# Kernel tuning notes

Hardware: AMD Instinct MI355X
Metric: run time of the kernel (lower is better)

The kernel has to match this reference:

```python
import jax, jax.numpy as jnp
import numpy as np

E = 1_600_000      # num edges
N = 50_000         # num nodes
G = 100            # num graphs in batch
EMB = 128          # emb_size
OUT = 256          # out_emb_size
NRAD = 6           # num_radial
NDENSE = 3         # num_dense


def setup_inputs() -> dict:
    key = jax.random.key(0)
    ks = jax.random.split(key, 8)
    m = jax.random.normal(ks[0], (E, EMB), dtype=jnp.float32)
    rbf = jax.random.normal(ks[1], (E, NRAD), dtype=jnp.float32)
    src = jax.random.randint(ks[2], (E,), 0, N, dtype=jnp.int64)
    graph_ids = jnp.sort(jax.random.randint(ks[3], (N,), 0, G, dtype=jnp.int64))
    # parameters (torch Linear convention: W [out, in])
    W_rbf = jax.random.normal(ks[4], (EMB, NRAD), dtype=jnp.float32) / np.sqrt(NRAD)
    W_up = jax.random.normal(ks[5], (OUT, EMB), dtype=jnp.float32) / np.sqrt(EMB)
    W_dense = jax.random.normal(ks[6], (NDENSE, OUT, OUT), dtype=jnp.float32) / np.sqrt(OUT)
    b_dense = jnp.zeros((NDENSE, OUT), dtype=jnp.float32)
    return {"m": m, "rbf": rbf, "src": src, "graph_ids": graph_ids,
            "W_rbf": W_rbf, "W_up": W_up, "W_dense": W_dense, "b_dense": b_dense}


def reference(m, rbf, src, graph_ids, W_rbf, W_up, W_dense, b_dense):
    # edge transform: tmp = m * dense_rbf(rbf)            [E, EMB]
    tmp = m * jnp.einsum('er,fr->ef', rbf, W_rbf)
    # reverse-graph copy_e/sum == scatter-sum onto original src nodes
    t = jax.ops.segment_sum(tmp, src, num_segments=N)     # [N, EMB]
    # up projection (no bias)
    t = jnp.einsum('ne,oe->no', t, W_up)                  # [N, OUT]
    # dense MLP with SiLU
    for i in range(NDENSE):
        t = jax.nn.silu(jnp.einsum('no,po->np', t, W_dense[i]) + b_dense[i])
    # extensive readout: per-graph sum
    out = jax.ops.segment_sum(t, graph_ids, num_segments=G)  # [G, OUT]
    return out
```

## Files before the change

### kernel.cpp

```cpp
#include <hip/hip_runtime.h>
#include <hip/hip_bf16.h>

typedef __attribute__((ext_vector_type(8))) short short8;
typedef __attribute__((ext_vector_type(4))) float f32x4;

#define EMB 128
#define OUT 256
#define NRAD 6
#define NDENSE 3
#define BSH 7
#define MAXBKT 512
#define HB 256

static __device__ __forceinline__ unsigned short f32_to_bf16(float f) {
    union { float f; unsigned u; } v; v.f = f;
    unsigned r = v.u + 0x7fffu + ((v.u >> 16) & 1u);
    return (unsigned short)(r >> 16);
}
static __device__ __forceinline__ float bf16_to_f32(unsigned short h) {
    union { unsigned u; float f; } v; v.u = ((unsigned)h) << 16;
    return v.f;
}
static __device__ __forceinline__ float silu(float x) {
    return x / (1.f + __expf(-x));
}
static __device__ __forceinline__ void gload_lds16(const void* gp, void* lp) {
    __builtin_amdgcn_global_load_lds(
        (const __attribute__((address_space(1))) void*)gp,
        (__attribute__((address_space(3))) void*)lp, 16, 0, 0);
}

__global__ __launch_bounds__(256) void init_kernel(
        const float* __restrict__ Wup, const float* __restrict__ Wd,
        unsigned short* __restrict__ Wbf, float* __restrict__ out, int outn) {
    int i = blockIdx.x * blockDim.x + threadIdx.x;
    int stride = gridDim.x * blockDim.x;
    for (int j = i; j < outn; j += stride) out[j] = 0.f;
    const int n1 = OUT * EMB, n2 = NDENSE * OUT * OUT;
    for (int j = i; j < n1 + n2; j += stride)
        Wbf[j] = f32_to_bf16(j < n1 ? Wup[j] : Wd[j - n1]);
}

__global__ __launch_bounds__(256) void bhist_kernel(
        const int* __restrict__ src, int* __restrict__ bpart, int E, int nbkt) {
    __shared__ int h[MAXBKT];
    for (int b = threadIdx.x; b < nbkt; b += 256) h[b] = 0;
    __syncthreads();
    int stride = gridDim.x * blockDim.x;
    for (int e = blockIdx.x * blockDim.x + threadIdx.x; e < E; e += stride)
        atomicAdd(&h[src[e] >> BSH], 1);
    __syncthreads();
    int* row = bpart + (size_t)blockIdx.x * MAXBKT;
    for (int b = threadIdx.x; b < nbkt; b += 256) row[b] = h[b];
}

__global__ __launch_bounds__(512) void bscan_kernel(
        const int* __restrict__ bpart, int* __restrict__ bbase,
        int* __restrict__ gcursor, int nbkt, int E) {
    __shared__ int s[MAXBKT];
    int t = threadIdx.x;
    int v = 0;
    if (t < nbkt)
        for (int k = 0; k < HB; ++k) v += bpart[(size_t)k * MAXBKT + t];
    s[t] = v;
    __syncthreads();
    for (int d = 1; d < MAXBKT; d <<= 1) {
        int x = (t >= d) ? s[t - d] : 0;
        __syncthreads();
        s[t] += x;
        __syncthreads();
    }
    if (t < nbkt) {
        int ex = s[t] - v;
        bbase[t] = ex;
        gcursor[t] = ex;
    }
    if (t == 0) bbase[nbkt] = E;
}

__global__ __launch_bounds__(256) void bscatter_kernel(
        const int* __restrict__ src, int* __restrict__ gcursor,
        int2* __restrict__ pairs, int E, int nbkt) {
    __shared__ int h[MAXBKT];
    __shared__ int base[MAXBKT];
    for (int b = threadIdx.x; b < nbkt; b += 256) h[b] = 0;
    __syncthreads();
    const int per = (E + gridDim.x - 1) / gridDim.x;
    const int e0 = blockIdx.x * per;
    const int e1 = min(e0 + per, E);
    for (int e = e0 + threadIdx.x; e < e1; e += 256)
        atomicAdd(&h[src[e] >> BSH], 1);
    __syncthreads();
    for (int b = threadIdx.x; b < nbkt; b += 256)
        base[b] = h[b] ? atomicAdd(&gcursor[b], h[b]) : 0;
    __syncthreads();
    for (int e = e0 + threadIdx.x; e < e1; e += 256) {
        int s = src[e];
        int pos = atomicAdd(&base[s >> BSH], 1);
        pairs[pos] = make_int2(e, s);
    }
}

__global__ __launch_bounds__(256) void local_csr_kernel(
        const int2* __restrict__ pairs, const int* __restrict__ bbase,
        int* __restrict__ offsets, int* __restrict__ perm, int N, int E, int nbkt) {
    __shared__ int cnt[128], exc[128], cur[128];
    const int b = blockIdx.x;
    const int t = threadIdx.x;
    const int n0 = b << BSH;
    const int nn = min(128, N - n0);
    const int p0 = bbase[b], p1 = bbase[b + 1];
    if (t < 128) cnt[t] = 0;
    __syncthreads();
    for (int i = p0 + t; i < p1; i += 256)
        atomicAdd(&cnt[pairs[i].y - n0], 1);
    __syncthreads();
    if (t < 128) exc[t] = cnt[t];
    __syncthreads();
    for (int d = 1; d < 128; d <<= 1) {
        int x = (t >= d && t < 128) ? exc[t - d] : 0;
        __syncthreads();
        if (t < 128) exc[t] += x;
        __syncthreads();
    }
    if (t < 128) {
        int ex = exc[t] - cnt[t];
        cur[t] = ex;
        if (t < nn) offsets[n0 + t] = p0 + ex;
    }
    if (b == 0 && t == 0) offsets[N] = E;
    __syncthreads();
    for (int i = p0 + t; i < p1; i += 256) {
        int2 pr = pairs[i];
        int pos = p0 + atomicAdd(&cur[pr.y - n0], 1);
        perm[pos] = pr.x;
    }
}

__global__ __launch_bounds__(256) void edge_accum_kernel(
        const float* __restrict__ m, const float* __restrict__ rbf,
        const int* __restrict__ perm, const int* __restrict__ offsets,
        const float* __restrict__ W_rbf, uint2* __restrict__ t_pack, int N) {
    const int lane = threadIdx.x & 63;
    const int h = lane >> 5;
    const int c = lane & 31;
    const int gw = blockIdx.x * (blockDim.x >> 6) + (threadIdx.x >> 6);
    const int nwaves = gridDim.x * (blockDim.x >> 6);

    float wk[4][6];
#pragma unroll
    for (int k = 0; k < 4; ++k)
#pragma unroll
        for (int j = 0; j < 6; ++j) wk[k][j] = W_rbf[(4 * c + k) * NRAD + j];

    for (int node = gw; node < N; node += nwaves) {
        const int beg = offsets[node], end = offsets[node + 1];
        float a0 = 0.f, a1 = 0.f, a2 = 0.f, a3 = 0.f;
        int pe = 0;
        if (beg < end) {
            int pi = beg + (lane & 15); if (pi > end - 1) pi = end - 1;
            pe = perm[pi];
        }
        for (int cb = beg; cb < end; cb += 16) {
            int pe_next = 0;
            if (cb + 16 < end) {
                int pi = cb + 16 + (lane & 15); if (pi > end - 1) pi = end - 1;
                pe_next = perm[pi];
            }
#pragma unroll
            for (int p = 0; p < 8; ++p) {
                int e = __shfl(pe, 2 * p + h);
                const float2* rp = (const float2*)(rbf + (size_t)e * NRAD);
                float2 r0 = rp[0], r1 = rp[1], r2 = rp[2];
                float4 mv = *(const float4*)(m + (size_t)e * EMB + 4 * c);
                float g = (cb + 2 * p + h < end) ? 1.f : 0.f;
                float p0 = (wk[0][0]*r0.x + wk[0][1]*r0.y + wk[0][2]*r1.x
                          + wk[0][3]*r1.y + wk[0][4]*r2.x + wk[0][5]*r2.y) * g;
                float p1 = (wk[1][0]*r0.x + wk[1][1]*r0.y + wk[1][2]*r1.x
                          + wk[1][3]*r1.y + wk[1][4]*r2.x + wk[1][5]*r2.y) * g;
                float p2 = (wk[2][0]*r0.x + wk[2][1]*r0.y + wk[2][2]*r1.x
                          + wk[2][3]*r1.y + wk[2][4]*r2.x + wk[2][5]*r2.y) * g;
                float p3 = (wk[3][0]*r0.x + wk[3][1]*r0.y + wk[3][2]*r1.x
                          + wk[3][3]*r1.y + wk[3][4]*r2.x + wk[3][5]*r2.y) * g;
                a0 = fmaf(mv.x, p0, a0);
                a1 = fmaf(mv.y, p1, a1);
                a2 = fmaf(mv.z, p2, a2);
                a3 = fmaf(mv.w, p3, a3);
            }
            pe = pe_next;
        }
        a0 += __shfl_xor(a0, 32);
        a1 += __shfl_xor(a1, 32);
        a2 += __shfl_xor(a2, 32);
        a3 += __shfl_xor(a3, 32);
        if (h == 0) {
            uint2 pk;
            pk.x = (unsigned)f32_to_bf16(a0) | ((unsigned)f32_to_bf16(a1) << 16);
            pk.y = (unsigned)f32_to_bf16(a2) | ((unsigned)f32_to_bf16(a3) << 16);
            t_pack[(size_t)node * 32 + c] = pk;
        }
    }
}

template<int K, int ACT>
__global__ __launch_bounds__(256) void gemm2_kernel(
        const unsigned short* __restrict__ A, const unsigned short* __restrict__ W,
        const float* __restrict__ bias, unsigned short* __restrict__ C, int M) {
    __shared__ char lds[32768];
    char* As = lds;
    char* Ws = lds + 16384;

    const int w    = threadIdx.x >> 6;
    const int lane = threadIdx.x & 63;
    const int r    = lane & 15;
    const int g    = lane >> 4;
    const int wr   = w >> 1;
    const int wc   = w & 1;
    const int row0 = blockIdx.x * 128;
    const int col0 = blockIdx.y * 128;

    f32x4 acc[4][4];
#pragma unroll
    for (int i = 0; i < 4; ++i)
#pragma unroll
        for (int j = 0; j < 4; ++j) acc[i][j] = (f32x4){0.f, 0.f, 0.f, 0.f};

    const int lrow = (lane >> 3);
    const int cdst = (lane & 7) * 16;

    for (int kc = 0; kc < K; kc += 64) {
        if (kc) __syncthreads();
#pragma unroll
        for (int it = 0; it < 4; ++it) {
            int slot = it * 4 + w;
            int row  = slot * 8 + lrow;
            int csrc = cdst ^ ((row & 7) << 4);
            int ga   = row0 + row; if (ga >= M) ga = M - 1;
            gload_lds16((const char*)A + ((size_t)ga * K + kc) * 2 + csrc,
                        As + slot * 1024);
            int gw_  = col0 + row;
            gload_lds16((const char*)W + ((size_t)gw_ * K + kc) * 2 + csrc,
                        Ws + slot * 1024);
        }
        asm volatile("s_waitcnt vmcnt(0)" ::: "memory");
        __syncthreads();

#pragma unroll
        for (int ks = 0; ks < 2; ++ks) {
            short8 af[4], bf[4];
#pragma unroll
            for (int mi = 0; mi < 4; ++mi) {
                int row = wr * 64 + mi * 16 + r;
                int byte = row * 128 + ks * 64 + g * 16;
                byte ^= (r & 7) << 4;
                af[mi] = *(const short8*)(As + byte);
            }
#pragma unroll
            for (int nj = 0; nj < 4; ++nj) {
                int col = wc * 64 + nj * 16 + r;
                int byte = col * 128 + ks * 64 + g * 16;
                byte ^= (r & 7) << 4;
                bf[nj] = *(const short8*)(Ws + byte);
            }
#pragma unroll
            for (int mi = 0; mi < 4; ++mi)
#pragma unroll
                for (int nj = 0; nj < 4; ++nj)
                    acc[mi][nj] = __builtin_amdgcn_mfma_f32_16x16x32_bf16(
                        af[mi], bf[nj], acc[mi][nj], 0, 0, 0);
        }
    }

#pragma unroll
    for (int nj = 0; nj < 4; ++nj) {
        int gcol = col0 + wc * 64 + nj * 16 + r;
        float b = bias ? bias[gcol] : 0.f;
#pragma unroll
        for (int mi = 0; mi < 4; ++mi) {
#pragma unroll
            for (int q = 0; q < 4; ++q) {
                int grow = row0 + wr * 64 + mi * 16 + g * 4 + q;
                if (grow < M) {
                    float x = acc[mi][nj][q] + b;
                    if (ACT) x = silu(x);
                    C[(size_t)grow * OUT + gcol] = f32_to_bf16(x);
                }
            }
        }
    }
}

__global__ __launch_bounds__(256) void graph_partial_kernel(
        const unsigned short* __restrict__ h, const int* __restrict__ gids,
        float* __restrict__ out, int M) {
    int gph = blockIdx.x, s = blockIdx.y;
    int c = threadIdx.x;
    int lo = 0, hi = M;
    while (lo < hi) { int mid = (lo + hi) >> 1; if (gids[mid] < gph) lo = mid + 1; else hi = mid; }
    int lo2 = lo, hi2 = M;
    while (lo2 < hi2) { int mid = (lo2 + hi2) >> 1; if (gids[mid] < gph + 1) lo2 = mid + 1; else hi2 = mid; }
    int len = lo2 - lo;
    int q = (len + 3) >> 2;
    int b0 = lo + s * q;
    int b1 = b0 + q; if (b1 > lo2) b1 = lo2;
    float a0 = 0.f, a1 = 0.f;
    int n = b0;
    for (; n + 1 < b1; n += 2) {
        a0 += bf16_to_f32(h[(size_t)n * OUT + c]);
        a1 += bf16_to_f32(h[(size_t)(n + 1) * OUT + c]);
    }
    for (; n < b1; ++n) a0 += bf16_to_f32(h[(size_t)n * OUT + c]);
    float v = a0 + a1;
    if (b0 < b1) atomicAdd(&out[(size_t)gph * OUT + c], v);
}

extern "C" void kernel_launch(void* const* d_in, const int* in_sizes, int n_in,
                              void* d_out, int out_size, void* d_ws, size_t ws_size,
                              hipStream_t stream) {
    const float* m         = (const float*)d_in[0];
    const float* rbf       = (const float*)d_in[1];
    const int*   src       = (const int*)d_in[2];
    const int*   gids      = (const int*)d_in[3];
    const float* W_rbf     = (const float*)d_in[4];
    const float* W_up      = (const float*)d_in[5];
    const float* W_dense   = (const float*)d_in[6];
    const float* b_dense   = (const float*)d_in[7];
    float* out = (float*)d_out;

    const int E = in_sizes[2];
    const int N = in_sizes[3];
    const int G = out_size / OUT;
    const int nbkt = (N + 127) >> BSH;

    size_t off = 0;
    auto alloc = [&](size_t bytes) -> void* {
        void* p = (char*)d_ws + off;
        off += (bytes + 255) & ~(size_t)255;
        return p;
    };
    int* bpart   = (int*)alloc((size_t)HB * MAXBKT * 4);
    int* bbase   = (int*)alloc((size_t)(MAXBKT + 1) * 4);
    int* gcursor = (int*)alloc((size_t)MAXBKT * 4);
    int* offsets = (int*)alloc(((size_t)N + 1) * 4);
    int2* pairs  = (int2*)alloc((size_t)E * 8);
    int* perm    = (int*)alloc((size_t)E * 4);
    unsigned short* t_bf = (unsigned short*)alloc((size_t)N * EMB * 2);
    unsigned short* h0   = (unsigned short*)alloc((size_t)N * OUT * 2);
    unsigned short* h1   = (unsigned short*)alloc((size_t)N * OUT * 2);
    unsigned short* Wbf  = (unsigned short*)alloc((size_t)(OUT * EMB + NDENSE * OUT * OUT) * 2);
    unsigned short* Wup_bf = Wbf;
    unsigned short* Wd_bf  = Wbf + OUT * EMB;

    bhist_kernel<<<HB, 256, 0, stream>>>(src, bpart, E, nbkt);
    init_kernel<<<512, 256, 0, stream>>>(W_up, W_dense, Wbf, out, out_size);
    bscan_kernel<<<1, MAXBKT, 0, stream>>>(bpart, bbase, gcursor, nbkt, E);
    bscatter_kernel<<<512, 256, 0, stream>>>(src, gcursor, pairs, E, nbkt);
    local_csr_kernel<<<nbkt, 256, 0, stream>>>(pairs, bbase, offsets, perm, N, E, nbkt);

    edge_accum_kernel<<<2048, 256, 0, stream>>>(m, rbf, perm, offsets, W_rbf,
                                                (uint2*)t_bf, N);

    dim3 ggrid((N + 127) / 128, 2);
    gemm2_kernel<EMB, 0><<<ggrid, 256, 0, stream>>>(t_bf, Wup_bf, nullptr, h0, N);
    gemm2_kernel<OUT, 1><<<ggrid, 256, 0, stream>>>(h0, Wd_bf + 0 * OUT * OUT, b_dense + 0 * OUT, h1, N);
    gemm2_kernel<OUT, 1><<<ggrid, 256, 0, stream>>>(h1, Wd_bf + 1 * OUT * OUT, b_dense + 1 * OUT, h0, N);
    gemm2_kernel<OUT, 1><<<ggrid, 256, 0, stream>>>(h0, Wd_bf + 2 * OUT * OUT, b_dense + 2 * OUT, h1, N);

    graph_partial_kernel<<<dim3(G, 4), 256, 0, stream>>>(h1, gids, out, N);
}
```

Measured before the change: 450.8 us.

## Fuse local CSR build and edge accumulation into bucketed LDS-atomic accumulation

Replaces the per-bucket CSR construction and the per-node gather-accumulate kernel with one kernel per 128-node bucket. Each block walks that bucket's (edge, src) pairs and accumulates m*rbf-projection into a 64 KB shared-memory tile using LDS float atomics, then writes bf16 results. This drops the perm/offsets arrays and a kernel launch, at the cost of only 391 blocks with large LDS (low occupancy, under 2 waves per CU) and atomic contention. It also unrolls the bucket-scan reduction loop.

```diff
diff --git a/kernel.cpp b/kernel.cpp
--- a/kernel.cpp
+++ b/kernel.cpp
@@ -60,8 +60,10 @@
     __shared__ int s[MAXBKT];
     int t = threadIdx.x;
     int v = 0;
-    if (t < nbkt)
+    if (t < nbkt) {
+#pragma unroll 8
         for (int k = 0; k < HB; ++k) v += bpart[(size_t)k * MAXBKT + t];
+    }
     s[t] = v;
     __syncthreads();
     for (int d = 1; d < MAXBKT; d <<= 1) {
@@ -101,104 +103,64 @@
     }
 }
 
-__global__ __launch_bounds__(256) void local_csr_kernel(
+__global__ __launch_bounds__(256) void bucket_accum_kernel(
+        const float* __restrict__ m, const float* __restrict__ rbf,
         const int2* __restrict__ pairs, const int* __restrict__ bbase,
-        int* __restrict__ offsets, int* __restrict__ perm, int N, int E, int nbkt) {
-    __shared__ int cnt[128], exc[128], cur[128];
+        const float* __restrict__ W_rbf, uint2* __restrict__ t_pack, int N) {
+    __shared__ float acc[128 * 128];
+    const int t = threadIdx.x;
     const int b = blockIdx.x;
-    const int t = threadIdx.x;
     const int n0 = b << BSH;
     const int nn = min(128, N - n0);
     const int p0 = bbase[b], p1 = bbase[b + 1];
-    if (t < 128) cnt[t] = 0;
-    __syncthreads();
-    for (int i = p0 + t; i < p1; i += 256)
-        atomicAdd(&cnt[pairs[i].y - n0], 1);
-    __syncthreads();
-    if (t < 128) exc[t] = cnt[t];
-    __syncthreads();
-    for (int d = 1; d < 128; d <<= 1) {
-        int x = (t >= d && t < 128) ? exc[t - d] : 0;
-        __syncthreads();
-        if (t < 128) exc[t] += x;
-        __syncthreads();
-    }
-    if (t < 128) {
-        int ex = exc[t] - cnt[t];
-        cur[t] = ex;
-        if (t < nn) offsets[n0 + t] = p0 + ex;
-    }
-    if (b == 0 && t == 0) offsets[N] = E;
-    __syncthreads();
-    for (int i = p0 + t; i < p1; i += 256) {
-        int2 pr = pairs[i];
-        int pos = p0 + atomicAdd(&cur[pr.y - n0], 1);
-        perm[pos] = pr.x;
-    }
-}
-
-__global__ __launch_bounds__(256) void edge_accum_kernel(
-        const float* __restrict__ m, const float* __restrict__ rbf,
-        const int* __restrict__ perm, const int* __restrict__ offsets,
-        const float* __restrict__ W_rbf, uint2* __restrict__ t_pack, int N) {
-    const int lane = threadIdx.x & 63;
-    const int h = lane >> 5;
-    const int c = lane & 31;
-    const int gw = blockIdx.x * (blockDim.x >> 6) + (threadIdx.x >> 6);
-    const int nwaves = gridDim.x * (blockDim.x >> 6);
+    const int c  = t & 31;
+    const int g8 = t >> 5;
+
+    for (int i = t; i < 128 * 128; i += 256) acc[i] = 0.f;
 
     float wk[4][6];
 #pragma unroll
     for (int k = 0; k < 4; ++k)
 #pragma unroll
-        for (int j = 0; j < 6; ++j) wk[k][j] = W_rbf[(4 * c + k) * NRAD + j];
-
-    for (int node = gw; node < N; node += nwaves) {
-        const int beg = offsets[node], end = offsets[node + 1];
-        float a0 = 0.f, a1 = 0.f, a2 = 0.f, a3 = 0.f;
-        int pe = 0;
-        if (beg < end) {
-            int pi = beg + (lane & 15); if (pi > end - 1) pi = end - 1;
-            pe = perm[pi];
-        }
-        for (int cb = beg; cb < end; cb += 16) {
-            int pe_next = 0;
-            if (cb + 16 < end) {
-                int pi = cb + 16 + (lane & 15); if (pi > end - 1) pi = end - 1;
-                pe_next = perm[pi];
+        for (int j = 0; j < 6; ++j) wk[k][j] = W_rbf[(c + 32 * k) * NRAD + j];
+    __syncthreads();
+
+    for (int i = p0; i < p1; i += 32) {
+        int2 pr[4]; float2 r[4][3]; float mv[4][4]; bool val[4];
+#pragma unroll
+        for (int u = 0; u < 4; ++u) {
+            int idx = i + u * 8 + g8;
+            val[u] = idx < p1;
+            int2 p = val[u] ? pairs[idx] : make_int2(0, n0);
+            pr[u] = p;
+            const float2* rp = (const float2*)(rbf + (size_t)p.x * NRAD);
+            r[u][0] = rp[0]; r[u][1] = rp[1]; r[u][2] = rp[2];
+            const float* mrow = m + (size_t)p.x * EMB;
+#pragma unroll
+            for (int k = 0; k < 4; ++k) mv[u][k] = mrow[c + 32 * k];
+        }
+#pragma unroll
+        for (int u = 0; u < 4; ++u) {
+            if (!val[u]) continue;
+            float* arow = acc + (pr[u].y - n0) * 128;
+#pragma unroll
+            for (int k = 0; k < 4; ++k) {
+                float p = wk[k][0]*r[u][0].x + wk[k][1]*r[u][0].y
+                        + wk[k][2]*r[u][1].x + wk[k][3]*r[u][1].y
+                        + wk[k][4]*r[u][2].x + wk[k][5]*r[u][2].y;
+                atomicAdd(&arow[c + 32 * k], mv[u][k] * p);
             }
-#pragma unroll
-            for (int p = 0; p < 8; ++p) {
-                int e = __shfl(pe, 2 * p + h);
-                const float2* rp = (const float2*)(rbf + (size_t)e * NRAD);
-                float2 r0 = rp[0], r1 = rp[1], r2 = rp[2];
-                float4 mv = *(const float4*)(m + (size_t)e * EMB + 4 * c);
-                float g = (cb + 2 * p + h < end) ? 1.f : 0.f;
-                float p0 = (wk[0][0]*r0.x + wk[0][1]*r0.y + wk[0][2]*r1.x
-                          + wk[0][3]*r1.y + wk[0][4]*r2.x + wk[0][5]*r2.y) * g;
-                float p1 = (wk[1][0]*r0.x + wk[1][1]*r0.y + wk[1][2]*r1.x
-                          + wk[1][3]*r1.y + wk[1][4]*r2.x + wk[1][5]*r2.y) * g;
-                float p2 = (wk[2][0]*r0.x + wk[2][1]*r0.y + wk[2][2]*r1.x
-                          + wk[2][3]*r1.y + wk[2][4]*r2.x + wk[2][5]*r2.y) * g;
-                float p3 = (wk[3][0]*r0.x + wk[3][1]*r0.y + wk[3][2]*r1.x
-                          + wk[3][3]*r1.y + wk[3][4]*r2.x + wk[3][5]*r2.y) * g;
-                a0 = fmaf(mv.x, p0, a0);
-                a1 = fmaf(mv.y, p1, a1);
-                a2 = fmaf(mv.z, p2, a2);
-                a3 = fmaf(mv.w, p3, a3);
-            }
-            pe = pe_next;
-        }
-        a0 += __shfl_xor(a0, 32);
-        a1 += __shfl_xor(a1, 32);
-        a2 += __shfl_xor(a2, 32);
-        a3 += __shfl_xor(a3, 32);
-        if (h == 0) {
-            uint2 pk;
-            pk.x = (unsigned)f32_to_bf16(a0) | ((unsigned)f32_to_bf16(a1) << 16);
-            pk.y = (unsigned)f32_to_bf16(a2) | ((unsigned)f32_to_bf16(a3) << 16);
-            t_pack[(size_t)node * 32 + c] = pk;
-        }
+        }
+    }
+    __syncthreads();
+
+    for (int idx = t; idx < nn * 32; idx += 256) {
+        int node = idx >> 5, cc = idx & 31;
+        const float* ap = acc + node * 128 + 4 * cc;
+        uint2 pk;
+        pk.x = (unsigned)f32_to_bf16(ap[0]) | ((unsigned)f32_to_bf16(ap[1]) << 16);
+        pk.y = (unsigned)f32_to_bf16(ap[2]) | ((unsigned)f32_to_bf16(ap[3]) << 16);
+        t_pack[(size_t)(n0 + node) * 32 + cc] = pk;
     }
 }
 
@@ -341,9 +303,7 @@
     int* bpart   = (int*)alloc((size_t)HB * MAXBKT * 4);
     int* bbase   = (int*)alloc((size_t)(MAXBKT + 1) * 4);
     int* gcursor = (int*)alloc((size_t)MAXBKT * 4);
-    int* offsets = (int*)alloc(((size_t)N + 1) * 4);
     int2* pairs  = (int2*)alloc((size_t)E * 8);
-    int* perm    = (int*)alloc((size_t)E * 4);
     unsigned short* t_bf = (unsigned short*)alloc((size_t)N * EMB * 2);
     unsigned short* h0   = (unsigned short*)alloc((size_t)N * OUT * 2);
     unsigned short* h1   = (unsigned short*)alloc((size_t)N * OUT * 2);
@@ -355,10 +315,9 @@
     init_kernel<<<512, 256, 0, stream>>>(W_up, W_dense, Wbf, out, out_size);
     bscan_kernel<<<1, MAXBKT, 0, stream>>>(bpart, bbase, gcursor, nbkt, E);
     bscatter_kernel<<<512, 256, 0, stream>>>(src, gcursor, pairs, E, nbkt);
-    local_csr_kernel<<<nbkt, 256, 0, stream>>>(pairs, bbase, offsets, perm, N, E, nbkt);
-
-    edge_accum_kernel<<<2048, 256, 0, stream>>>(m, rbf, perm, offsets, W_rbf,
-                                                (uint2*)t_bf, N);
+
+    bucket_accum_kernel<<<nbkt, 256, 0, stream>>>(m, rbf, pairs, bbase, W_rbf,
+                                                  (uint2*)t_bf, N);
 
     dim3 ggrid((N + 127) / 128, 2);
     gemm2_kernel<EMB, 0><<<ggrid, 256, 0, stream>>>(t_bf, Wup_bf, nullptr, h0, N);
```

After: 1.592 ms. +253.2%, slower.

## Fuse up-projection and dense MLP GEMMs into one kernel keeping activations in LDS

Applied to the files above, without the earlier changes.

Replaces the four separate GEMM launches (up projection plus three dense SiLU layers) with a single kernel. Each block owns 64 rows and keeps the full 256-wide intermediate activation in LDS across all layers, streaming only the weights. This removes the global writes and reads of the N×256 bf16 intermediates and three launches, but reloads every weight matrix per 64-row block and has no load/compute overlap. The bscan reduction loop is also given an unroll pragma.

```diff
diff --git a/kernel.cpp b/kernel.cpp
--- a/kernel.cpp
+++ b/kernel.cpp
@@ -60,8 +60,10 @@
     __shared__ int s[MAXBKT];
     int t = threadIdx.x;
     int v = 0;
-    if (t < nbkt)
+    if (t < nbkt) {
+#pragma unroll 8
         for (int k = 0; k < HB; ++k) v += bpart[(size_t)k * MAXBKT + t];
+    }
     s[t] = v;
     __syncthreads();
     for (int d = 1; d < MAXBKT; d <<= 1) {
@@ -202,65 +204,66 @@
     }
 }
 
-template<int K, int ACT>
-__global__ __launch_bounds__(256) void gemm2_kernel(
-        const unsigned short* __restrict__ A, const unsigned short* __restrict__ W,
-        const float* __restrict__ bias, unsigned short* __restrict__ C, int M) {
-    __shared__ char lds[32768];
-    char* As = lds;
-    char* Ws = lds + 16384;
-
-    const int w    = threadIdx.x >> 6;
-    const int lane = threadIdx.x & 63;
+__global__ __launch_bounds__(256) void fused_mlp2_kernel(
+        const unsigned short* __restrict__ A0,
+        const unsigned short* __restrict__ Wup,
+        const unsigned short* __restrict__ Wd,
+        const float* __restrict__ bd,
+        unsigned short* __restrict__ Hout, int M) {
+    __shared__ char Abuf[32768];
+    __shared__ char Wbuf[32768];
+    const int t    = threadIdx.x;
+    const int w    = t >> 6;
+    const int lane = t & 63;
     const int r    = lane & 15;
     const int g    = lane >> 4;
-    const int wr   = w >> 1;
-    const int wc   = w & 1;
-    const int row0 = blockIdx.x * 128;
-    const int col0 = blockIdx.y * 128;
+    const int row0 = blockIdx.x * 64;
 
     f32x4 acc[4][4];
+
+#pragma unroll
+    for (int it = 0; it < 4; ++it) {
+        int unit = it * 256 + t;
+        int row  = unit >> 4;
+        int seg  = unit & 15;
+        int csrc = (seg * 16) ^ ((row & 7) << 4);
+        int ga = row0 + row; if (ga >= M) ga = M - 1;
+        gload_lds16((const char*)A0 + (size_t)ga * 256 + csrc, Abuf + unit * 16);
+    }
+
 #pragma unroll
     for (int i = 0; i < 4; ++i)
 #pragma unroll
         for (int j = 0; j < 4; ++j) acc[i][j] = (f32x4){0.f, 0.f, 0.f, 0.f};
-
-    const int lrow = (lane >> 3);
-    const int cdst = (lane & 7) * 16;
-
-    for (int kc = 0; kc < K; kc += 64) {
-        if (kc) __syncthreads();
-#pragma unroll
-        for (int it = 0; it < 4; ++it) {
-            int slot = it * 4 + w;
-            int row  = slot * 8 + lrow;
-            int csrc = cdst ^ ((row & 7) << 4);
-            int ga   = row0 + row; if (ga >= M) ga = M - 1;
-            gload_lds16((const char*)A + ((size_t)ga * K + kc) * 2 + csrc,
-                        As + slot * 1024);
-            int gw_  = col0 + row;
-            gload_lds16((const char*)W + ((size_t)gw_ * K + kc) * 2 + csrc,
-                        Ws + slot * 1024);
+#pragma unroll
+    for (int kci = 0; kci < 2; ++kci) {
+        const int kc = kci * 64;
+        if (kci) __syncthreads();
+#pragma unroll
+        for (int it = 0; it < 8; ++it) {
+            int unit = it * 256 + t;
+            int wrow = unit >> 3;
+            int seg  = unit & 7;
+            int csrc = (seg * 16) ^ ((wrow & 7) << 4);
+            gload_lds16((const char*)Wup + (size_t)wrow * 256 + kc * 2 + csrc,
+                        Wbuf + unit * 16);
         }
         asm volatile("s_waitcnt vmcnt(0)" ::: "memory");
         __syncthreads();
-
 #pragma unroll
         for (int ks = 0; ks < 2; ++ks) {
             short8 af[4], bf[4];
 #pragma unroll
             for (int mi = 0; mi < 4; ++mi) {
-                int row = wr * 64 + mi * 16 + r;
-                int byte = row * 128 + ks * 64 + g * 16;
-                byte ^= (r & 7) << 4;
-                af[mi] = *(const short8*)(As + byte);
+                int row = mi * 16 + r;
+                int off = kc * 2 + ks * 64 + g * 16;
+                af[mi] = *(const short8*)(Abuf + row * 256 + (off ^ ((row & 7) << 4)));
             }
 #pragma unroll
             for (int nj = 0; nj < 4; ++nj) {
-                int col = wc * 64 + nj * 16 + r;
-                int byte = col * 128 + ks * 64 + g * 16;
-                byte ^= (r & 7) << 4;
-                bf[nj] = *(const short8*)(Ws + byte);
+                int col = w * 64 + nj * 16 + r;
+                bf[nj] = *(const short8*)(Wbuf + col * 128
+                          + ((ks * 64 + g * 16) ^ ((col & 7) << 4)));
             }
 #pragma unroll
             for (int mi = 0; mi < 4; ++mi)
@@ -270,21 +273,96 @@
                         af[mi], bf[nj], acc[mi][nj], 0, 0, 0);
         }
     }
-
-#pragma unroll
-    for (int nj = 0; nj < 4; ++nj) {
-        int gcol = col0 + wc * 64 + nj * 16 + r;
-        float b = bias ? bias[gcol] : 0.f;
-#pragma unroll
-        for (int mi = 0; mi < 4; ++mi) {
+    __syncthreads();
+#pragma unroll
+    for (int mi = 0; mi < 4; ++mi)
+#pragma unroll
+        for (int nj = 0; nj < 4; ++nj)
 #pragma unroll
             for (int q = 0; q < 4; ++q) {
-                int grow = row0 + wr * 64 + mi * 16 + g * 4 + q;
-                if (grow < M) {
-                    float x = acc[mi][nj][q] + b;
-                    if (ACT) x = silu(x);
-                    C[(size_t)grow * OUT + gcol] = f32_to_bf16(x);
+                int row = mi * 16 + g * 4 + q;
+                int col = w * 64 + nj * 16 + r;
+                *(unsigned short*)(Abuf + row * 512 + ((col * 2) ^ ((row & 7) << 4)))
+                    = f32_to_bf16(acc[mi][nj][q]);
+            }
+    __syncthreads();
+
+    for (int ell = 0; ell < NDENSE; ++ell) {
+        const unsigned short* Wl = Wd + (size_t)ell * OUT * OUT;
+        const float* bias = bd + ell * OUT;
+#pragma unroll
+        for (int i = 0; i < 4; ++i)
+#pragma unroll
+            for (int j = 0; j < 4; ++j) acc[i][j] = (f32x4){0.f, 0.f, 0.f, 0.f};
+#pragma unroll
+        for (int kci = 0; kci < 4; ++kci) {
+            const int kc = kci * 64;
+            __syncthreads();
+#pragma unroll
+            for (int it = 0; it < 8; ++it) {
+                int unit = it * 256 + t;
+                int wrow = unit >> 3;
+                int seg  = unit & 7;
+                int csrc = (seg * 16) ^ ((wrow & 7) << 4);
+                gload_lds16((const char*)Wl + (size_t)wrow * 512 + kc * 2 + csrc,
+                            Wbuf + unit * 16);
+            }
+            asm volatile("s_waitcnt vmcnt(0)" ::: "memory");
+            __syncthreads();
+#pragma unroll
+            for (int ks = 0; ks < 2; ++ks) {
+                short8 af[4], bf[4];
+#pragma unroll
+                for (int mi = 0; mi < 4; ++mi) {
+                    int row = mi * 16 + r;
+                    int off = kc * 2 + ks * 64 + g * 16;
+                    af[mi] = *(const short8*)(Abuf + row * 512 + (off ^ ((row & 7) << 4)));
                 }
+#pragma unroll
+                for (int nj = 0; nj < 4; ++nj) {
+                    int col = w * 64 + nj * 16 + r;
+                    bf[nj] = *(const short8*)(Wbuf + col * 128
+                              + ((ks * 64 + g * 16) ^ ((col & 7) << 4)));
+                }
+#pragma unroll
+                for (int mi = 0; mi < 4; ++mi)
+#pragma unroll
+                    for (int nj = 0; nj < 4; ++nj)
+                        acc[mi][nj] = __builtin_amdgcn_mfma_f32_16x16x32_bf16(
+                            af[mi], bf[nj], acc[mi][nj], 0, 0, 0);
+            }
+        }
+        __syncthreads();
+        if (ell < NDENSE - 1) {
+#pragma unroll
+            for (int mi = 0; mi < 4; ++mi)
+#pragma unroll
+                for (int nj = 0; nj < 4; ++nj) {
+                    int col = w * 64 + nj * 16 + r;
+                    float b = bias[col];
+#pragma unroll
+                    for (int q = 0; q < 4; ++q) {
+                        int row = mi * 16 + g * 4 + q;
+                        *(unsigned short*)(Abuf + row * 512
+                            + ((col * 2) ^ ((row & 7) << 4)))
+                            = f32_to_bf16(silu(acc[mi][nj][q] + b));
+                    }
+                }
+            __syncthreads();
+        } else {
+#pragma unroll
+            for (int nj = 0; nj < 4; ++nj) {
+                int gcol = w * 64 + nj * 16 + r;
+                float b = bias[gcol];
+#pragma unroll
+                for (int mi = 0; mi < 4; ++mi)
+#pragma unroll
+                    for (int q = 0; q < 4; ++q) {
+                        int grow = row0 + mi * 16 + g * 4 + q;
+                        if (grow < M)
+                            Hout[(size_t)grow * OUT + gcol]
+                                = f32_to_bf16(silu(acc[mi][nj][q] + b));
+                    }
             }
         }
     }
@@ -345,7 +423,6 @@
     int2* pairs  = (int2*)alloc((size_t)E * 8);
     int* perm    = (int*)alloc((size_t)E * 4);
     unsigned short* t_bf = (unsigned short*)alloc((size_t)N * EMB * 2);
-    unsigned short* h0   = (unsigned short*)alloc((size_t)N * OUT * 2);
     unsigned short* h1   = (unsigned short*)alloc((size_t)N * OUT * 2);
     unsigned short* Wbf  = (unsigned short*)alloc((size_t)(OUT * EMB + NDENSE * OUT * OUT) * 2);
     unsigned short* Wup_bf = Wbf;
@@ -360,11 +437,8 @@
     edge_accum_kernel<<<2048, 256, 0, stream>>>(m, rbf, perm, offsets, W_rbf,
                                                 (uint2*)t_bf, N);
 
-    dim3 ggrid((N + 127) / 128, 2);
-    gemm2_kernel<EMB, 0><<<ggrid, 256, 0, stream>>>(t_bf, Wup_bf, nullptr, h0, N);
-    gemm2_kernel<OUT, 1><<<ggrid, 256, 0, stream>>>(h0, Wd_bf + 0 * OUT * OUT, b_dense + 0 * OUT, h1, N);
-    gemm2_kernel<OUT, 1><<<ggrid, 256, 0, stream>>>(h1, Wd_bf + 1 * OUT * OUT, b_dense + 1 * OUT, h0, N);
-    gemm2_kernel<OUT, 1><<<ggrid, 256, 0, stream>>>(h0, Wd_bf + 2 * OUT * OUT, b_dense + 2 * OUT, h1, N);
+    fused_mlp2_kernel<<<(N + 63) / 64, 256, 0, stream>>>(t_bf, Wup_bf, Wd_bf,
+                                                         b_dense, h1, N);
 
     graph_partial_kernel<<<dim3(G, 4), 256, 0, stream>>>(h1, gids, out, N);
 }
```

Result: faster. 440.0 us (-2.4%).
